# Performance work log

Measured on AMD Instinct MI355X. Metric: run time of the kernel, lower is better.

## Reference

```python
import jax, jax.numpy as jnp
from jax import lax
import numpy as np

K = 32        # self.k: neighbors queried per center
TOP = 5       # inner topk size (hardcoded in source)
MAX_ITER = 16 # bound on the data-dependent while loop; leftovers emitted at final iter


def _refine_one(pc, centers, ids):
    """Vectorized translation of the per-batch while-loop.

    Instead of shrinking the sample set each iteration (data-dependent shape),
    every sample is tracked with an `active` flag and a convergence-iteration
    stamp. Emitting order in the torch code is (iteration, surviving-order),
    and boolean masking preserves relative original order, so a stable sort by
    (conv_iter, original_index) reproduces the exact concatenation order.
    """
    N, D = pc.shape
    S = centers.shape[0]
    ar = jnp.arange(S)

    def knn(q):  # q: [S,3] -> [S,K] indices of nearest cloud points (ascending dist)
        d2 = jnp.sum((q[:, None, :] - pc[None, :, :]) ** 2, axis=-1)  # [S,N]
        _, ind = lax.top_k(-d2, K)
        return ind

    def step(cur_pts, cur_idx):
        ind = knn(cur_pts)                                   # [S,K]
        nbh = pc[ind]                                        # [S,K,3]
        gc = jnp.mean(nbh, axis=1)                           # [S,3]
        dist = jnp.linalg.norm(nbh - gc[:, None, :], axis=2) # [S,K]
        _, top = lax.top_k(-dist, TOP)                       # [S,TOP] smallest dists
        in_top = jnp.any(top == 0, axis=1)                   # center (col 0) stable?
        new_idx = ind[ar, top[:, 0]]                         # point closest to centroid
        return ind, in_top, new_idx

    def body(it, st):
        cur_pts, cur_idx, conv_it, out_pts, out_idx, out_grp, active = st
        ind, in_top, new_idx = step(cur_pts, cur_idx)
        newly = active & in_top
        conv_it = jnp.where(newly, it, conv_it)
        out_pts = jnp.where(newly[:, None], cur_pts, out_pts)
        out_idx = jnp.where(newly, cur_idx, out_idx)
        out_grp = jnp.where(newly[:, None], ind, out_grp)
        move = active & ~in_top
        cur_idx = jnp.where(move, new_idx, cur_idx)
        cur_pts = jnp.where(move[:, None], pc[new_idx], cur_pts)
        return (cur_pts, cur_idx, conv_it, out_pts, out_idx, out_grp, move)

    st0 = (centers, ids,
           jnp.full((S,), MAX_ITER, jnp.int32),
           jnp.zeros((S, D), pc.dtype),
           jnp.zeros((S,), ids.dtype),
           jnp.zeros((S, K), jnp.int32),
           jnp.ones((S,), bool))
    cur_pts, cur_idx, conv_it, out_pts, out_idx, out_grp, active = lax.fori_loop(
        0, MAX_ITER, body, st0)

    # force-emit any sample that never converged within MAX_ITER
    ind, _, _ = step(cur_pts, cur_idx)
    out_pts = jnp.where(active[:, None], cur_pts, out_pts)
    out_idx = jnp.where(active, cur_idx, out_idx)
    out_grp = jnp.where(active[:, None], ind, out_grp)

    order = jnp.argsort(conv_it * (S + 1) + ar)  # stable (iter, orig-pos) order
    return out_pts[order], out_idx[order], out_grp[order]


def setup_inputs() -> dict:
    key = jax.random.key(0)
    k1, k2, k3 = jax.random.split(key, 3)
    B, N, S = 8, 8192, 1024
    xyz = jax.random.normal(k1, (B, N, 3), jnp.float32)
    center = jax.random.normal(k2, (B, S, 3), jnp.float32)
    idx = jax.random.randint(k3, (B, S), 0, N, jnp.int32)
    return {"xyz": xyz, "center": center, "idx": idx}


def reference(xyz, center, idx):
    assert xyz.shape[0] == center.shape[0]
    C, I1, I2 = jax.vmap(_refine_one)(xyz, center, idx)
    # torch runs under no_grad; outputs are detached constants
    return (lax.stop_gradient(C), I1, I2)
```

## Files before the change

kernel.cpp:

```cpp
#include <hip/hip_runtime.h>
#include <stdint.h>

#define BATCH   8
#define NPTS    8192
#define SCH     1024
#define KNN     32
#define TOPC    5
#define MAXIT   16
#define NCELL   4096
#define NGRP    128
#define NSEED   6
#define FCAP    128

typedef unsigned long long ull;
typedef float vf2 __attribute__((ext_vector_type(2)));
typedef float vf4 __attribute__((ext_vector_type(4)));

#define SENTKEY ((((ull)0x7F800000u) << 13) | 0x1FFFull)

#define ROTL(lane, g) (((lane) + (g) * 17) & 63)

__device__ __forceinline__ uint32_t xshfl32(uint32_t v, int xl) {
    if (xl == 1)
        return (uint32_t)__builtin_amdgcn_update_dpp((int)v, (int)v, 0xB1, 0xF, 0xF, true);
    if (xl == 2)
        return (uint32_t)__builtin_amdgcn_update_dpp((int)v, (int)v, 0x4E, 0xF, 0xF, true);
    return (uint32_t)__shfl_xor((int)v, xl, 64);
}
__device__ __forceinline__ ull xshfl64(ull v, int xl) {
    uint32_t lo = xshfl32((uint32_t)v, xl);
    uint32_t hi = xshfl32((uint32_t)(v >> 32), xl);
    return ((ull)hi << 32) | lo;
}
__device__ __forceinline__ float xshflf(float v, int xl) {
    return __uint_as_float(xshfl32(__float_as_uint(v), xl));
}

__device__ __forceinline__ float d2_exact(vf4 q, vf4 p) {
#pragma clang fp contract(off)
    vf2 d = q.xy - p.xy;
    vf2 s = d * d;
    float dz = q.z - p.z;
    float sz = dz * dz;
    return (s.x + s.y) + sz;
}

__device__ __forceinline__ void insert_top4(ull key, ull& k0, ull& k1, ull& k2,
                                            ull& k3, float& th) {
    if (key < k3) {
        k3 = key;
        { bool c = k3 < k2; ull mn = c ? k3 : k2, mx = c ? k2 : k3; k2 = mn; k3 = mx; }
        { bool c = k2 < k1; ull mn = c ? k2 : k1, mx = c ? k1 : k2; k1 = mn; k2 = mx; }
        { bool c = k1 < k0; ull mn = c ? k1 : k0, mx = c ? k0 : k1; k0 = mn; k1 = mx; }
        th = __uint_as_float((uint32_t)(k3 >> 13));
    }
}

__device__ __forceinline__ ull wave_min_u64(ull k) {
#pragma unroll
    for (int off = 32; off; off >>= 1) {
        ull o = xshfl64(k, off);
        k = o < k ? o : k;
    }
    return k;
}
__device__ __forceinline__ ull wave_max_u64(ull k) {
#pragma unroll
    for (int off = 32; off; off >>= 1) {
        ull o = xshfl64(k, off);
        k = o > k ? o : k;
    }
    return k;
}

__device__ __forceinline__ float bbox_mind2(vf4 q, vf4 c, vf4 h) {
    float dx = fmaxf(fabsf(q.x - c.x) - h.x, 0.f);
    float dy = fmaxf(fabsf(q.y - c.y) - h.y, 0.f);
    float dz = fmaxf(fabsf(q.z - c.z) - h.z, 0.f);
    return (dx * dx + dy * dy + dz * dz) * 0.9999f;
}

__device__ __forceinline__ ull cx(ull v, int xl, bool keepmin) {
    ull o = xshfl64(v, xl);
    return ((v < o) == keepmin) ? v : o;
}
__device__ __forceinline__ void cswap(ull& a, ull& b, bool up) {
    bool lt = a < b;
    ull mn = lt ? a : b, mx = lt ? b : a;
    a = up ? mn : mx;
    b = up ? mx : mn;
}

__device__ __forceinline__ uint32_t cx32(uint32_t v, int xl, bool keepmin) {
    uint32_t o = xshfl32(v, xl);
    return ((v < o) == keepmin) ? v : o;
}
__device__ __forceinline__ void cswap32(uint32_t& a, uint32_t& b, bool up) {
    uint32_t mn = a < b ? a : b, mx = a < b ? b : a;
    a = up ? mn : mx;
    b = up ? mx : mn;
}

__device__ __forceinline__ void sort128_u32(uint32_t& s0, uint32_t& s1, int lane) {
    cswap32(s0, s1, true);
    if (lane & 1) { uint32_t t = s0; s0 = s1; s1 = t; }
#pragma unroll
    for (int kk = 4; kk <= 128; kk <<= 1) {
        const bool up = (lane & (kk >> 1)) == 0;
#pragma unroll
        for (int d = kk >> 1; d >= 2; d >>= 1) {
            const int xl = d >> 1;
            const bool keepmin = (up == ((lane & xl) == 0));
            s0 = cx32(s0, xl, keepmin);
            s1 = cx32(s1, xl, keepmin);
        }
        cswap32(s0, s1, up);
    }
}

__device__ __forceinline__ void sort128_u64(ull& s0, ull& s1, int lane) {
    cswap(s0, s1, true);
    if (lane & 1) { ull t = s0; s0 = s1; s1 = t; }
#pragma unroll
    for (int kk = 4; kk <= 128; kk <<= 1) {
        const bool up = (lane & (kk >> 1)) == 0;
#pragma unroll
        for (int d = kk >> 1; d >= 2; d >>= 1) {
            const int xl = d >> 1;
            const bool keepmin = (up == ((lane & xl) == 0));
            s0 = cx(s0, xl, keepmin);
            s1 = cx(s1, xl, keepmin);
        }
        cswap(s0, s1, up);
    }
}

__device__ __forceinline__ int next_gid(ull& r0, ull& r1) {
    if (r0) { int g = __ffsll((unsigned long long)r0) - 1; r0 &= r0 - 1; return g; }
    if (r1) { int g = __ffsll((unsigned long long)r1) - 1; r1 &= r1 - 1; return 64 + g; }
    return -1;
}

__device__ __forceinline__ int cell_of(float x, float y, float z) {
    int cxi = min(15, max(0, (int)floorf((x + 4.0f) * 2.0f)));
    int cyi = min(15, max(0, (int)floorf((y + 4.0f) * 2.0f)));
    int czi = min(15, max(0, (int)floorf((z + 4.0f) * 2.0f)));
    uint32_t sx = (cxi & 1) | ((cxi & 2) << 2) | ((cxi & 4) << 4) | ((cxi & 8) << 6);
    uint32_t sy = (cyi & 1) | ((cyi & 2) << 2) | ((cyi & 4) << 4) | ((cyi & 8) << 6);
    uint32_t sz = (czi & 1) | ((czi & 2) << 2) | ((czi & 4) << 4) | ((czi & 8) << 6);
    return (int)(sx | (sy << 1) | (sz << 2));
}

__device__ __attribute__((noinline)) int serial_topk_masked(
    const vf4* __restrict__ Psort, vf4 q, int lane, ull sm0, ull sm1) {
    ull k0 = SENTKEY, k1 = SENTKEY, k2 = SENTKEY, k3 = SENTKEY;
    int s0 = 0, s1 = 0, s2 = 0, s3 = 0;
    float th = __builtin_inff();
    for (int gid = 0; gid < NGRP; ++gid) {
        bool sel = (gid < 64) ? ((sm0 >> gid) & 1ull) : ((sm1 >> (gid - 64)) & 1ull);
        if (!sel) continue;
        vf4 p = Psort[(gid << 6) + lane];
        float d2 = d2_exact(q, p);
        uint32_t oi = __float_as_uint(p.w);
        ull key = ((ull)__float_as_uint(d2) << 13) | oi;
        if (d2 <= th && key < k3) {
            k3 = key; s3 = gid;
            if (k3 < k2) { ull t = k2; k2 = k3; k3 = t; int ts = s2; s2 = s3; s3 = ts; }
            if (k2 < k1) { ull t = k1; k1 = k2; k2 = t; int ts = s1; s1 = s2; s2 = ts; }
            if (k1 < k0) { ull t = k0; k0 = k1; k1 = t; int ts = s0; s0 = s1; s1 = ts; }
            th = __uint_as_float((uint32_t)(k3 >> 13));
        }
    }
    ull em0 = 0ull, em1 = 0ull;
    int cnt = 4, my_ind = 0;
    for (int r = 0; r < KNN; ++r) {
        ull gmin = wave_min_u64(k0);
        int widx = (int)(gmin & 0x1FFFull);
        if (lane == r) my_ind = widx;
        if (k0 == gmin) {
            int g = s0;
            if (g < 64) em0 |= 1ull << g; else em1 |= 1ull << (g - 64);
            k0 = k1; k1 = k2; k2 = k3; k3 = SENTKEY;
            s0 = s1; s1 = s2; s2 = s3;
            if (--cnt == 0) {
                k0 = k1 = k2 = k3 = SENTKEY;
                float th2 = __builtin_inff();
                for (int gid = 0; gid < NGRP; ++gid) {
                    bool sel = (gid < 64) ? ((sm0 >> gid) & 1ull)
                                          : ((sm1 >> (gid - 64)) & 1ull);
                    bool ex = (gid < 64) ? ((em0 >> gid) & 1ull)
                                         : ((em1 >> (gid - 64)) & 1ull);
                    if (!sel || ex) continue;
                    vf4 p = Psort[(gid << 6) + lane];
                    float d2 = d2_exact(q, p);
                    uint32_t oi = __float_as_uint(p.w);
                    ull key = ((ull)__float_as_uint(d2) << 13) | oi;
                    if (d2 <= th2 && key < k3) {
                        k3 = key; s3 = gid;
                        if (k3 < k2) { ull t = k2; k2 = k3; k3 = t; int ts = s2; s2 = s3; s3 = ts; }
                        if (k2 < k1) { ull t = k1; k1 = k2; k2 = t; int ts = s1; s1 = s2; s2 = ts; }
                        if (k1 < k0) { ull t = k0; k0 = k1; k1 = t; int ts = s0; s0 = s1; s1 = ts; }
                        th2 = __uint_as_float((uint32_t)(k3 >> 13));
                    }
                }
                cnt = 4;
            }
        }
    }
    return my_ind;
}

__device__ int collect_topk(const vf4* __restrict__ Psort, vf4 q, int lane,
                            ull sm0, ull sm1, ull tau,
                            ull* buf, int* cnt) {
    if (lane == 0) *cnt = 0;
    __asm__ volatile("s_waitcnt lgkmcnt(0)" ::: "memory");
    ull r0 = sm0, r1 = sm1;
    int g = next_gid(r0, r1);
    while (g >= 0) {
        vf4 p = Psort[(g << 6) + lane];
        float d2 = d2_exact(q, p);
        ull key = ((ull)__float_as_uint(d2) << 13) | __float_as_uint(p.w);
        if (key <= tau) {
            int pos = atomicAdd(cnt, 1);
            if (pos < FCAP) buf[pos] = key;
        }
        g = next_gid(r0, r1);
    }
    __asm__ volatile("s_waitcnt lgkmcnt(0)" ::: "memory");
    const int M = *cnt;
    if (M > FCAP) return -1;
    ull s0 = (2 * lane + 0 < M) ? buf[2 * lane + 0] : SENTKEY;
    ull s1 = (2 * lane + 1 < M) ? buf[2 * lane + 1] : SENTKEY;
    sort128_u64(s0, s1, lane);
    const int src = lane >> 1;
    const uint32_t e0 = (uint32_t)__shfl((int)(uint32_t)s0, src, 64);
    const uint32_t e1 = (uint32_t)__shfl((int)(uint32_t)s1, src, 64);
    return (int)(((lane & 1) ? e1 : e0) & 0x1FFFu);
}

__global__ __launch_bounds__(256) void prep_kernel(const float* __restrict__ xyz,
                                                   vf4* __restrict__ pc4,
                                                   int* __restrict__ counts) {
    int i = (int)(blockIdx.x * blockDim.x + threadIdx.x);
    if (i >= BATCH * NPTS) return;
    vf4 v;
    v.x = xyz[(size_t)i * 3 + 0];
    v.y = xyz[(size_t)i * 3 + 1];
    v.z = xyz[(size_t)i * 3 + 2];
    v.w = 0.f;
    pc4[i] = v;
    int b = i >> 13;
    atomicAdd(&counts[b * NCELL + cell_of(v.x, v.y, v.z)], 1);
}

__global__ __launch_bounds__(1024) void sortbuild_kernel(
    const vf4* __restrict__ pc4, const int* __restrict__ counts,
    vf4* __restrict__ sortedP, vf4* __restrict__ bC, vf4* __restrict__ bH) {
    const int b = (int)blockIdx.x;
    const int t = (int)threadIdx.x, lane = t & 63, w = t >> 6;
    __shared__ int cur[NCELL];
    __shared__ int wsum[16];

    const int base = t * 4;
    const int gb = b * NCELL + base;
    const int v0 = counts[gb], v1 = counts[gb + 1], v2 = counts[gb + 2], v3 = counts[gb + 3];
    const int s = v0 + v1 + v2 + v3;
    int incl = s;
#pragma unroll
    for (int off = 1; off < 64; off <<= 1) {
        int o = __shfl_up(incl, off, 64);
        if (lane >= off) incl += o;
    }
    if (lane == 63) wsum[w] = incl;
    __syncthreads();
    if (t == 0) {
        int acc = 0;
#pragma unroll
        for (int i = 0; i < 16; ++i) { int x = wsum[i]; wsum[i] = acc; acc += x; }
    }
    __syncthreads();
    const int excl = incl - s + wsum[w];
    cur[base]     = excl;
    cur[base + 1] = excl + v0;
    cur[base + 2] = excl + v0 + v1;
    cur[base + 3] = excl + v0 + v1 + v2;
    __syncthreads();

#pragma unroll
    for (int k = 0; k < 8; ++k) {
        const int i = k * 1024 + t;
        vf4 v = pc4[((size_t)b << 13) + i];
        const int c = cell_of(v.x, v.y, v.z);
        const int pos = atomicAdd(&cur[c], 1);
        v.w = __uint_as_float((uint32_t)i);
        sortedP[((size_t)b << 13) + pos] = v;
    }
    __syncthreads();

    for (int g = w; g < NGRP; g += 16) {
        vf4 p = sortedP[((size_t)b << 13) + (g << 6) + lane];
        float mnx = p.x, mxx = p.x, mny = p.y, mxy = p.y, mnz = p.z, mxz = p.z;
#pragma unroll
        for (int off = 32; off; off >>= 1) {
            mnx = fminf(mnx, xshflf(mnx, off));
            mxx = fmaxf(mxx, xshflf(mxx, off));
            mny = fminf(mny, xshflf(mny, off));
            mxy = fmaxf(mxy, xshflf(mxy, off));
            mnz = fminf(mnz, xshflf(mnz, off));
            mxz = fmaxf(mxz, xshflf(mxz, off));
        }
        if (lane == 0) {
            vf4 c, h;
            c.x = (mnx + mxx) * 0.5f; c.y = (mny + mxy) * 0.5f; c.z = (mnz + mxz) * 0.5f; c.w = 0.f;
            h.x = (mxx - mnx) * 0.5f; h.y = (mxy - mny) * 0.5f; h.z = (mxz - mnz) * 0.5f; h.w = 0.f;
            bC[(b << 7) + g] = c;
            bH[(b << 7) + g] = h;
        }
    }
}

__global__ __launch_bounds__(256)
__attribute__((amdgpu_waves_per_eu(2, 4)))
void refine_kernel(
    const vf4* __restrict__ pc4, const vf4* __restrict__ sortedP,
    const vf4* __restrict__ bC, const vf4* __restrict__ bH,
    const float* __restrict__ center, const int* __restrict__ idx_in,
    float* __restrict__ pts_ws, int* __restrict__ idx_ws,
    int* __restrict__ grp_ws, int* __restrict__ conv_ws) {
    const int lane = (int)(threadIdx.x & 63);
    const int w = (int)(threadIdx.x >> 6);
    const int b = (int)(blockIdx.x & 7);
    const int s = (((int)blockIdx.x >> 3) << 2) + w;
    const vf4* __restrict__ Porig = pc4 + ((size_t)b << 13);
    const vf4* __restrict__ Psort = sortedP + ((size_t)b << 13);

    __shared__ vf4 sbC[NGRP], sbH[NGRP];
    __shared__ vf4 nbh[4][KNN];
    __shared__ ull fbuf[4][FCAP];
    __shared__ int fcnt[4];

    {
        const int t = (int)threadIdx.x;
        if (t < NGRP) sbC[t] = bC[(b << 7) + t];
        else          sbH[t - NGRP] = bH[(b << 7) + (t - NGRP)];
    }
    __syncthreads();

    const size_t ch = ((size_t)b << 10) + (size_t)s;
    vf4 q;
    q.x = center[ch * 3 + 0];
    q.y = center[ch * 3 + 1];
    q.z = center[ch * 3 + 2];
    q.w = 0.f;
    int qidx = idx_in[ch];

    int conv = MAXIT;
    int my_ind = 0;
    vf4 myp = q;
    bool warm = false;

    for (int it = 0;; ++it) {
        const vf4 c0 = sbC[lane],      h0 = sbH[lane];
        const vf4 c1 = sbC[64 + lane], h1 = sbH[64 + lane];
        const float m0 = bbox_mind2(q, c0, h0);
        const float m1 = bbox_mind2(q, c1, h1);

        ull k0 = SENTKEY, k1 = SENTKEY, k2 = SENTKEY, k3 = SENTKEY;
        float th = __builtin_inff();
        ull sm0 = 0ull, sm1 = 0ull, am0 = 0ull, am1 = 0ull;
        float th0 = __builtin_inff();

        bool fastwarm = false;
        if (warm) {
            const float dw = (lane < KNN) ? d2_exact(q, myp) : 0.f;
            th0 = dw;
#pragma unroll
            for (int off = 32; off; off >>= 1)
                th0 = fmaxf(th0, xshflf(th0, off));
            sm0 = __ballot(m0 <= th0);
            sm1 = __ballot(m1 <= th0);
            const int nsel = __popcll(sm0) + __popcll(sm1);
            if (nsel <= 20) { fastwarm = true; am0 = sm0; am1 = sm1; }
        }

        if (!fastwarm) {
            sm0 = 0ull; sm1 = 0ull;
            uint32_t g0k = ((__float_as_uint(m0) >> 6) << 7) | (uint32_t)lane;
            uint32_t g1k = ((__float_as_uint(m1) >> 6) << 7) | (uint32_t)(64 + lane);
            sort128_u32(g0k, g1k, lane);
#pragma unroll
            for (int r = 0; r < NSEED; ++r) {
                const uint32_t nk = (r & 1)
                    ? (uint32_t)__shfl((int)g1k, r >> 1, 64)
                    : (uint32_t)__shfl((int)g0k, r >> 1, 64);
                const int gid = (int)(nk & 127u);
                if (gid < 64) sm0 |= 1ull << gid; else sm1 |= 1ull << (gid - 64);
                const vf4 p = Psort[(gid << 6) + ROTL(lane, gid)];
                const float d2 = d2_exact(q, p);
                if (d2 <= th)
                    insert_top4(((ull)__float_as_uint(d2) << 13) | __float_as_uint(p.w),
                                k0, k1, k2, k3, th);
            }
            ull t = k0;
            {
                ull o = xshfl64(t, 32);
                t = o < t ? o : t;
            }
            const ull B = wave_max_u64(t);
            const float Bd = fminf(__uint_as_float((uint32_t)(B >> 13)), th0);
            am0 = __ballot(m0 <= Bd) & ~sm0;
            am1 = __ballot(m1 <= Bd) & ~sm1;
            sm0 |= am0; sm1 |= am1;
        }

        {
            ull rem0 = am0, rem1 = am1;
            int ga = next_gid(rem0, rem1);
            while (ga >= 0) {
                const int gb2 = next_gid(rem0, rem1);
                const vf4 pa = Psort[(ga << 6) + ROTL(lane, ga)];
                vf4 pb;
                if (gb2 >= 0) pb = Psort[(gb2 << 6) + ROTL(lane, gb2)];
                const float da = d2_exact(q, pa);
                if (da <= th)
                    insert_top4(((ull)__float_as_uint(da) << 13) | __float_as_uint(pa.w),
                                k0, k1, k2, k3, th);
                if (gb2 >= 0) {
                    const float dbv = d2_exact(q, pb);
                    if (dbv <= th)
                        insert_top4(((ull)__float_as_uint(dbv) << 13) | __float_as_uint(pb.w),
                                    k0, k1, k2, k3, th);
                }
                ga = next_gid(rem0, rem1);
            }
        }
        const ull prek3 = k3;

        const bool odd = (lane & 1) != 0;
        ull a0 = odd ? k3 : k0;
        ull a1 = odd ? k2 : k1;
        ull a2 = odd ? k1 : k2;
        ull a3 = odd ? k0 : k3;
#pragma unroll
        for (int kk = 8; kk <= 256; kk <<= 1) {
            const bool up = (lane & (kk >> 2)) == 0;
#pragma unroll
            for (int d = kk >> 1; d >= 4; d >>= 1) {
                const int xl = d >> 2;
                const bool keepmin = (up == ((lane & xl) == 0));
                a0 = cx(a0, xl, keepmin);
                a1 = cx(a1, xl, keepmin);
                a2 = cx(a2, xl, keepmin);
                a3 = cx(a3, xl, keepmin);
            }
            cswap(a0, a2, up); cswap(a1, a3, up);
            cswap(a0, a1, up); cswap(a2, a3, up);
        }
        const ull tau = (ull)__shfl((unsigned long long)a3, 7, 64);
        const ull bad = __ballot(prek3 < tau);
        if (bad != 0ull) {
            const int mi = collect_topk(Psort, q, lane, sm0, sm1, tau,
                                        fbuf[w], &fcnt[w]);
            my_ind = (mi >= 0) ? mi : serial_topk_masked(Psort, q, lane, sm0, sm1);
        } else {
            const int src = lane >> 2;
            const uint32_t lo0 = (uint32_t)__shfl((int)(uint32_t)a0, src, 64);
            const uint32_t lo1 = (uint32_t)__shfl((int)(uint32_t)a1, src, 64);
            const uint32_t lo2 = (uint32_t)__shfl((int)(uint32_t)a2, src, 64);
            const uint32_t lo3 = (uint32_t)__shfl((int)(uint32_t)a3, src, 64);
            const int sel = lane & 3;
            uint32_t lo = (sel == 0) ? lo0 : (sel == 1) ? lo1 : (sel == 2) ? lo2 : lo3;
            my_ind = (int)(lo & 0x1FFFu);
        }

        if (it == MAXIT) break;

        myp = q;
        if (lane < KNN) {
            myp = Porig[my_ind];
            nbh[w][lane] = myp;
        }
        __asm__ volatile("s_waitcnt lgkmcnt(0)" ::: "memory");
        float sx = 0.f, sy = 0.f, sz = 0.f;
#pragma unroll
        for (int j = 0; j < KNN; ++j) {
            vf4 pj = nbh[w][j];
            sx = __fadd_rn(sx, pj.x);
            sy = __fadd_rn(sy, pj.y);
            sz = __fadd_rn(sz, pj.z);
        }
        const float gx = __fmul_rn(sx, 0.03125f);
        const float gy = __fmul_rn(sy, 0.03125f);
        const float gz = __fmul_rn(sz, 0.03125f);

        float dj = __builtin_inff();
        if (lane < KNN) {
            const float dx = __fsub_rn(myp.x, gx);
            const float dy = __fsub_rn(myp.y, gy);
            const float dz = __fsub_rn(myp.z, gz);
            dj = sqrtf(__fadd_rn(__fadd_rn(__fmul_rn(dx, dx), __fmul_rn(dy, dy)),
                                 __fmul_rn(dz, dz)));
        }
        const uint32_t db = __float_as_uint(dj);
        const uint32_t d0 = (uint32_t)__shfl((int)db, 0, 64);
        const ull bal = __ballot(db < d0);
        if (__popcll(bal) <= TOPC - 1) { conv = it; break; }

        uint32_t m = db;
#pragma unroll
        for (int off = 32; off; off >>= 1) {
            uint32_t o = xshfl32(m, off);
            m = o < m ? o : m;
        }
        const ull balm = __ballot(db == m);
        const int jm = __ffsll((unsigned long long)balm) - 1;
        qidx = __shfl(my_ind, jm, 64);
        q.x = __shfl(myp.x, jm, 64);
        q.y = __shfl(myp.y, jm, 64);
        q.z = __shfl(myp.z, jm, 64);
        q.w = 0.f;
        warm = true;
    }

    if (lane < KNN) grp_ws[ch * KNN + lane] = my_ind;
    if (lane == 0) {
        pts_ws[ch * 3 + 0] = q.x;
        pts_ws[ch * 3 + 1] = q.y;
        pts_ws[ch * 3 + 2] = q.z;
        idx_ws[ch] = qidx;
        conv_ws[ch] = conv;
    }
}

__global__ __launch_bounds__(1024) void order_kernel(
    const float* __restrict__ pts_ws, const int* __restrict__ idx_ws,
    const int* __restrict__ grp_ws, const int* __restrict__ conv_ws,
    float* __restrict__ out) {
    const int b = (int)blockIdx.x;
    const int s = (int)threadIdx.x;
    const int w = s >> 6, l = s & 63;
    __shared__ int wavecnt[16][MAXIT + 1];
    __shared__ int binbase[MAXIT + 1];
    const size_t ch = (size_t)b * SCH + s;
    const int c = conv_ws[ch];
    int rw = 0;
#pragma unroll
    for (int v = 0; v <= MAXIT; ++v) {
        ull bal = __ballot(c == v);
        if (l == 0) wavecnt[w][v] = (int)__popcll(bal);
        if (c == v) rw = (int)__popcll(bal & ((1ull << l) - 1ull));
    }
    __syncthreads();
    if (s == 0) {
        int acc = 0;
        for (int v = 0; v <= MAXIT; ++v) {
            int t = 0;
            for (int w2 = 0; w2 < 16; ++w2) t += wavecnt[w2][v];
            binbase[v] = acc;
            acc += t;
        }
    }
    __syncthreads();
    int pos = binbase[c] + rw;
    for (int w2 = 0; w2 < w; ++w2) pos += wavecnt[w2][c];

    float* __restrict__ C  = out;
    float* __restrict__ I1 = out + (size_t)BATCH * SCH * 3;
    float* __restrict__ I2 = I1 + (size_t)BATCH * SCH;
    const size_t o = (size_t)b * SCH + pos;
    C[o * 3 + 0] = pts_ws[ch * 3 + 0];
    C[o * 3 + 1] = pts_ws[ch * 3 + 1];
    C[o * 3 + 2] = pts_ws[ch * 3 + 2];
    I1[o] = (float)idx_ws[ch];
#pragma unroll
    for (int k = 0; k < KNN; ++k) I2[o * KNN + k] = (float)grp_ws[ch * KNN + k];
}

extern "C" void kernel_launch(void* const* d_in, const int* in_sizes, int n_in,
                              void* d_out, int out_size, void* d_ws, size_t ws_size,
                              hipStream_t stream) {
    const float* xyz    = (const float*)d_in[0];
    const float* center = (const float*)d_in[1];
    const int*   idx_in = (const int*)d_in[2];
    float* out = (float*)d_out;

    char* wp = (char*)d_ws;
    vf4* pc4     = (vf4*)wp;  wp += (size_t)BATCH * NPTS * sizeof(vf4);
    vf4* sortedP = (vf4*)wp;  wp += (size_t)BATCH * NPTS * sizeof(vf4);
    vf4* bC      = (vf4*)wp;  wp += (size_t)BATCH * NGRP * sizeof(vf4);
    vf4* bH      = (vf4*)wp;  wp += (size_t)BATCH * NGRP * sizeof(vf4);
    int* counts  = (int*)wp;  wp += (size_t)BATCH * NCELL * 4;
    float* pts_ws = (float*)wp; wp += (size_t)BATCH * SCH * 3 * 4;
    int*   idx_ws = (int*)wp;   wp += (size_t)BATCH * SCH * 4;
    int*   grp_ws = (int*)wp;   wp += (size_t)BATCH * SCH * KNN * 4;
    int*   conv_ws = (int*)wp;

    hipMemsetAsync(counts, 0, (size_t)BATCH * NCELL * 4, stream);
    prep_kernel<<<(BATCH * NPTS + 255) / 256, 256, 0, stream>>>(xyz, pc4, counts);
    sortbuild_kernel<<<BATCH, 1024, 0, stream>>>(pc4, counts, sortedP, bC, bH);

    const int chains = BATCH * SCH;
    refine_kernel<<<chains * 64 / 256, 256, 0, stream>>>(
        pc4, sortedP, bC, bH, center, idx_in, pts_ws, idx_ws, grp_ws, conv_ws);
    order_kernel<<<BATCH, SCH, 0, stream>>>(pts_ws, idx_ws, grp_ws, conv_ws, out);
}
```

Before: 188.6 us.

## Split 8-block sort/build kernel into scan, scatter and bbox kernels

The single sortbuild kernel ran on only 8 blocks, one per batch, doing the prefix scan, LDS-atomic scatter and per-group bounding boxes serially inside each block. It is replaced by three kernels: a per-batch scan writing cursors to global memory, a grid-wide scatter using global atomics, and a grid-wide bbox reduction. This spreads the scatter and bbox work across many CUs. In exchange it adds two kernel launches, and the scatter now uses global instead of LDS atomics. Point order within a cell still depends on atomic order.

```diff
diff --git a/kernel.cpp b/kernel.cpp
--- a/kernel.cpp
+++ b/kernel.cpp
@@ -254,18 +254,14 @@
     atomicAdd(&counts[b * NCELL + cell_of(v.x, v.y, v.z)], 1);
 }
 
-__global__ __launch_bounds__(1024) void sortbuild_kernel(
-    const vf4* __restrict__ pc4, const int* __restrict__ counts,
-    vf4* __restrict__ sortedP, vf4* __restrict__ bC, vf4* __restrict__ bH) {
-    const int b = (int)blockIdx.x;
-    const int t = (int)threadIdx.x, lane = t & 63, w = t >> 6;
-    __shared__ int cur[NCELL];
+__global__ __launch_bounds__(1024) void scan_kernel(const int* __restrict__ counts,
+                                                    int* __restrict__ cursor) {
+    int b = (int)blockIdx.x, tid = (int)threadIdx.x;
+    int lane = tid & 63, w = tid >> 6;
     __shared__ int wsum[16];
-
-    const int base = t * 4;
-    const int gb = b * NCELL + base;
-    const int v0 = counts[gb], v1 = counts[gb + 1], v2 = counts[gb + 2], v3 = counts[gb + 3];
-    const int s = v0 + v1 + v2 + v3;
+    int base = b * NCELL + tid * 4;
+    int v0 = counts[base], v1 = counts[base + 1], v2 = counts[base + 2], v3 = counts[base + 3];
+    int s = v0 + v1 + v2 + v3;
     int incl = s;
 #pragma unroll
     for (int off = 1; off < 64; off <<= 1) {
@@ -274,49 +270,54 @@
     }
     if (lane == 63) wsum[w] = incl;
     __syncthreads();
-    if (t == 0) {
+    if (tid == 0) {
         int acc = 0;
 #pragma unroll
         for (int i = 0; i < 16; ++i) { int x = wsum[i]; wsum[i] = acc; acc += x; }
     }
     __syncthreads();
-    const int excl = incl - s + wsum[w];
-    cur[base]     = excl;
-    cur[base + 1] = excl + v0;
-    cur[base + 2] = excl + v0 + v1;
-    cur[base + 3] = excl + v0 + v1 + v2;
-    __syncthreads();
-
-#pragma unroll
-    for (int k = 0; k < 8; ++k) {
-        const int i = k * 1024 + t;
-        vf4 v = pc4[((size_t)b << 13) + i];
-        const int c = cell_of(v.x, v.y, v.z);
-        const int pos = atomicAdd(&cur[c], 1);
-        v.w = __uint_as_float((uint32_t)i);
-        sortedP[((size_t)b << 13) + pos] = v;
-    }
-    __syncthreads();
-
-    for (int g = w; g < NGRP; g += 16) {
-        vf4 p = sortedP[((size_t)b << 13) + (g << 6) + lane];
-        float mnx = p.x, mxx = p.x, mny = p.y, mxy = p.y, mnz = p.z, mxz = p.z;
-#pragma unroll
-        for (int off = 32; off; off >>= 1) {
-            mnx = fminf(mnx, xshflf(mnx, off));
-            mxx = fmaxf(mxx, xshflf(mxx, off));
-            mny = fminf(mny, xshflf(mny, off));
-            mxy = fmaxf(mxy, xshflf(mxy, off));
-            mnz = fminf(mnz, xshflf(mnz, off));
-            mxz = fmaxf(mxz, xshflf(mxz, off));
-        }
-        if (lane == 0) {
-            vf4 c, h;
-            c.x = (mnx + mxx) * 0.5f; c.y = (mny + mxy) * 0.5f; c.z = (mnz + mxz) * 0.5f; c.w = 0.f;
-            h.x = (mxx - mnx) * 0.5f; h.y = (mxy - mny) * 0.5f; h.z = (mxz - mnz) * 0.5f; h.w = 0.f;
-            bC[(b << 7) + g] = c;
-            bH[(b << 7) + g] = h;
-        }
+    int excl = incl - s + wsum[w];
+    cursor[base]     = excl;
+    cursor[base + 1] = excl + v0;
+    cursor[base + 2] = excl + v0 + v1;
+    cursor[base + 3] = excl + v0 + v1 + v2;
+}
+
+__global__ __launch_bounds__(256) void scatter_kernel(const vf4* __restrict__ pc4,
+                                                      int* __restrict__ cursor,
+                                                      vf4* __restrict__ sortedP) {
+    int i = (int)(blockIdx.x * blockDim.x + threadIdx.x);
+    if (i >= BATCH * NPTS) return;
+    vf4 v = pc4[i];
+    int b = i >> 13, pi = i & (NPTS - 1);
+    int c = cell_of(v.x, v.y, v.z);
+    int pos = atomicAdd(&cursor[b * NCELL + c], 1);
+    v.w = __uint_as_float((uint32_t)pi);
+    sortedP[((size_t)b << 13) + pos] = v;
+}
+
+__global__ __launch_bounds__(256) void bbox_kernel(const vf4* __restrict__ sortedP,
+                                                   vf4* __restrict__ bC,
+                                                   vf4* __restrict__ bH) {
+    int g = (int)((blockIdx.x * blockDim.x + threadIdx.x) >> 6);
+    int lane = (int)(threadIdx.x & 63);
+    vf4 p = sortedP[((size_t)g << 6) + lane];
+    float mnx = p.x, mxx = p.x, mny = p.y, mxy = p.y, mnz = p.z, mxz = p.z;
+#pragma unroll
+    for (int off = 32; off; off >>= 1) {
+        mnx = fminf(mnx, xshflf(mnx, off));
+        mxx = fmaxf(mxx, xshflf(mxx, off));
+        mny = fminf(mny, xshflf(mny, off));
+        mxy = fmaxf(mxy, xshflf(mxy, off));
+        mnz = fminf(mnz, xshflf(mnz, off));
+        mxz = fmaxf(mxz, xshflf(mxz, off));
+    }
+    if (lane == 0) {
+        vf4 c, h;
+        c.x = (mnx + mxx) * 0.5f; c.y = (mny + mxy) * 0.5f; c.z = (mnz + mxz) * 0.5f; c.w = 0.f;
+        h.x = (mxx - mnx) * 0.5f; h.y = (mxy - mny) * 0.5f; h.z = (mxz - mnz) * 0.5f; h.w = 0.f;
+        bC[g] = c;
+        bH[g] = h;
     }
 }
 
@@ -591,6 +592,7 @@
     vf4* bC      = (vf4*)wp;  wp += (size_t)BATCH * NGRP * sizeof(vf4);
     vf4* bH      = (vf4*)wp;  wp += (size_t)BATCH * NGRP * sizeof(vf4);
     int* counts  = (int*)wp;  wp += (size_t)BATCH * NCELL * 4;
+    int* cursor  = (int*)wp;  wp += (size_t)BATCH * NCELL * 4;
     float* pts_ws = (float*)wp; wp += (size_t)BATCH * SCH * 3 * 4;
     int*   idx_ws = (int*)wp;   wp += (size_t)BATCH * SCH * 4;
     int*   grp_ws = (int*)wp;   wp += (size_t)BATCH * SCH * KNN * 4;
@@ -598,7 +600,9 @@
 
     hipMemsetAsync(counts, 0, (size_t)BATCH * NCELL * 4, stream);
     prep_kernel<<<(BATCH * NPTS + 255) / 256, 256, 0, stream>>>(xyz, pc4, counts);
-    sortbuild_kernel<<<BATCH, 1024, 0, stream>>>(pc4, counts, sortedP, bC, bH);
+    scan_kernel<<<BATCH, 1024, 0, stream>>>(counts, cursor);
+    scatter_kernel<<<(BATCH * NPTS + 255) / 256, 256, 0, stream>>>(pc4, cursor, sortedP);
+    bbox_kernel<<<(BATCH * NGRP * 64) / 256, 256, 0, stream>>>(sortedP, bC, bH);
 
     const int chains = BATCH * SCH;
     refine_kernel<<<chains * 64 / 256, 256, 0, stream>>>(
```

Result: faster. 180.8 us (median of 2 runs) (-4.1%).
